# Performance work log

Measured on AMD Instinct MI355X. Metric: run time of the kernel, lower is better.

The kernel has to match this reference:

```python
import jax, jax.numpy as jnp
import numpy as np

N_NODES = 100000


def gcn_conv(x, W, b, src, dst, n):
    # PyG GCNConv: add self-loops, symmetric deg^-1/2 normalization,
    # transform then gather/scatter-add aggregate.
    loop = jnp.arange(n, dtype=src.dtype)
    s = jnp.concatenate([src, loop])
    d = jnp.concatenate([dst, loop])
    deg = jax.ops.segment_sum(jnp.ones_like(d, dtype=x.dtype), d, num_segments=n)
    dinv = jnp.where(deg > 0, 1.0 / jnp.sqrt(deg), 0.0)
    norm = dinv[s] * dinv[d]                      # [E+N]
    h = x @ W                                     # [N, out]
    msgs = h[s] * norm[:, None]                   # gather + scale
    out = jax.ops.segment_sum(msgs, d, num_segments=n)  # scatter-add
    return out + b


def setup_inputs() -> dict:
    key = jax.random.key(0)
    k1, k2, k3, k4 = jax.random.split(key, 4)
    F_in, H, D = 128, 16, 128
    x = jax.random.normal(k1, (N_NODES, F_in), dtype=jnp.float32)
    edge_index = jax.random.randint(k2, (2, 1600000), 0, N_NODES, dtype=jnp.int64)
    W1 = jax.random.normal(k3, (F_in, H), dtype=jnp.float32) / np.sqrt(F_in)
    b1 = jnp.zeros((H,), dtype=jnp.float32)
    W2 = jax.random.normal(k4, (H, D), dtype=jnp.float32) / np.sqrt(H)
    b2 = jnp.zeros((D,), dtype=jnp.float32)
    return {"x": x, "edge_index": edge_index, "W1": W1, "b1": b1, "W2": W2, "b2": b2}


def reference(x, edge_index, W1, b1, W2, b2):
    src, dst = edge_index[0], edge_index[1]
    n = x.shape[0]
    h = jax.nn.relu(gcn_conv(x, W1, b1, src, dst, n))
    out = jax.nn.relu(gcn_conv(h, W2, b2, src, dst, n))
    return out
```

## Files before the change

### kernel.cpp

```cpp
#include <hip/hip_runtime.h>
#include <hip/hip_fp16.h>
#include <stdint.h>

#define F_IN  128
#define HID   16
#define F_OUT 128
#define NBK   512
#define NBLK  512
#define BCAP  4096
#define CHUNK_MAX 4096
#define EPT   16
#define XP1   132
#define GT2_NODES 128

__device__ __forceinline__ int bucket_of(int d, int N) {
    return (int)(((long long)d * NBK) / N);
}
__device__ __forceinline__ int bucket_lo(int b, int N) {
    return (int)(((long long)b * N + NBK - 1) / NBK);
}

__global__ void __launch_bounds__(256) k_partf(
        const int* __restrict__ ei, int* __restrict__ bcur,
        uint32_t* __restrict__ pairs, int E, int N) {
    __shared__ int lh[NBK], lofs[NBK], lcur[NBK], gbase[NBK], lnlo[NBK];
    __shared__ int loff[256];
    __shared__ uint32_t spairs[CHUNK_MAX];
    __shared__ uint16_t sbkt[CHUNK_MAX];

    int blk = blockIdx.x, t = threadIdx.x;
    int C = (E + NBLK - 1) / NBLK;
    int e0 = blk * C;
    int e1 = e0 + C; if (e1 > E) e1 = E;
    int ecnt = e1 - e0;

    for (int i = t; i < NBK; i += 256) { lh[i] = 0; lnlo[i] = bucket_lo(i, N); }
    __syncthreads();

    int es[EPT], ed[EPT], eb[EPT];
#pragma unroll
    for (int k = 0; k < EPT; ++k) {
        int e = e0 + k * 256 + t;
        if (e < e1) {
            es[k] = ei[e];
            ed[k] = ei[E + e];
            eb[k] = bucket_of(ed[k], N);
            atomicAdd(&lh[eb[k]], 1);
        } else eb[k] = -1;
    }
    __syncthreads();

    int a0 = lh[2 * t], a1 = lh[2 * t + 1];
    int s2 = a0 + a1;
    loff[t] = s2;
    __syncthreads();
    for (int o = 1; o < 256; o <<= 1) {
        int a = (t >= o) ? loff[t - o] : 0;
        __syncthreads();
        loff[t] += a;
        __syncthreads();
    }
    int excl = loff[t] - s2;
    lofs[2 * t]     = excl;
    lofs[2 * t + 1] = excl + a0;
    lcur[2 * t]     = excl;
    lcur[2 * t + 1] = excl + a0;
    __syncthreads();

    for (int w = 0; w < NBK; w += 256) {
        int i = (t + w + blk) & (NBK - 1);
        int h = lh[i];
        gbase[i] = h ? atomicAdd(&bcur[i], h) : 0;
    }

#pragma unroll
    for (int k = 0; k < EPT; ++k) {
        if (eb[k] >= 0) {
            int b = eb[k];
            int idx = atomicAdd(&lcur[b], 1);
            spairs[idx] = ((uint32_t)es[k] << 10) | (uint32_t)(ed[k] - lnlo[b]);
            sbkt[idx]   = (uint16_t)b;
        }
    }
    __syncthreads();

    for (int i = t; i < ecnt; i += 256) {
        int b = sbkt[i];
        int pos = gbase[b] + (i - lofs[b]);
        if (pos < BCAP)
            pairs[(size_t)b * BCAP + pos] = spairs[i];
    }
}

__global__ void __launch_bounds__(256) k_csr_t1(
        const uint32_t* __restrict__ pairs, const int* __restrict__ bcur,
        const float* __restrict__ x, const float* __restrict__ W1,
        int* __restrict__ row_start, int* __restrict__ cnt,
        float* __restrict__ dinv, int* __restrict__ srcs,
        __half* __restrict__ g1, int N) {
    __shared__ union {
        struct { int lcnt[256]; int loff[256]; int lcur[256]; } c;
        struct { float sX[32 * XP1]; float sWt[HID * XP1]; } t1;
    } u;
    __shared__ float sdinv[224];

    int b = blockIdx.x, t = threadIdx.x;
    int base = b * BCAP;
    int ec = bcur[b]; if (ec > BCAP) ec = BCAP;
    int nlo = bucket_lo(b, N);
    int nhi = bucket_lo(b + 1, N); if (nhi > N) nhi = N;
    int nn = nhi - nlo;

    u.c.lcnt[t] = 0;
    __syncthreads();
    for (int e = t; e < ec; e += 256)
        atomicAdd(&u.c.lcnt[pairs[base + e] & 1023u], 1);
    __syncthreads();
    int v = u.c.lcnt[t];
    int pv = (v + 3) & ~3;
    u.c.loff[t] = pv;
    __syncthreads();
    for (int o = 1; o < 256; o <<= 1) {
        int a = (t >= o) ? u.c.loff[t - o] : 0;
        __syncthreads();
        u.c.loff[t] += a;
        __syncthreads();
    }
    if (t < nn) {
        int gs = base + (u.c.loff[t] - pv);
        row_start[nlo + t] = gs;
        cnt[nlo + t]       = v;
        float dv = rsqrtf((float)(v + 1));
        dinv[nlo + t]      = dv;
        sdinv[t]           = dv;
        u.c.lcur[t]        = gs;
    }
    __syncthreads();
    for (int e = t; e < ec; e += 256) {
        uint32_t p = pairs[base + e];
        int pos = atomicAdd(&u.c.lcur[p & 1023u], 1);
        srcs[pos] = (int)(p >> 10);
    }
    __syncthreads();

    for (int i = t; i < F_IN * HID; i += 256) {
        int k = i >> 4, f = i & 15;
        u.t1.sWt[f * XP1 + k] = W1[i];
    }
    int f  = t & 7;
    int nl = t >> 3;
    for (int c0 = 0; c0 < nn; c0 += 32) {
        __syncthreads();
        int node0 = nlo + c0;
        int nrem = nn - c0;
        const float4* x4 = (const float4*)(x + (size_t)node0 * F_IN);
#pragma unroll
        for (int j = 0; j < 4; ++j) {
            int idx4 = t + j * 256;
            int nl2 = idx4 >> 5;
            int kk = (idx4 & 31) * 4;
            float4 vv = make_float4(0.f, 0.f, 0.f, 0.f);
            if (nl2 < nrem) vv = x4[idx4];
            *(float4*)&u.t1.sX[nl2 * XP1 + kk] = vv;
        }
        __syncthreads();
        float a0 = 0.f, a1 = 0.f;
        const float* xr  = &u.t1.sX[nl * XP1];
        const float* wr0 = &u.t1.sWt[f * XP1];
        const float* wr1 = &u.t1.sWt[(f + 8) * XP1];
#pragma unroll 4
        for (int k = 0; k < F_IN; k += 4) {
            float4 xv = *(const float4*)(xr + k);
            float4 w0 = *(const float4*)(wr0 + k);
            float4 w1 = *(const float4*)(wr1 + k);
            a0 += xv.x * w0.x + xv.y * w0.y + xv.z * w0.z + xv.w * w0.w;
            a1 += xv.x * w1.x + xv.y * w1.y + xv.z * w1.z + xv.w * w1.w;
        }
        if (nl < nrem) {
            int node = node0 + nl;
            float di = sdinv[c0 + nl];
            g1[(size_t)node * HID + f]     = __float2half(di * a0);
            g1[(size_t)node * HID + f + 8] = __float2half(di * a1);
        }
    }
}

__device__ __forceinline__ void add_h8(float* __restrict__ acc, const __half* __restrict__ ptr) {
    uint4 u = *(const uint4*)ptr;
    const __half2* h = (const __half2*)&u;
#pragma unroll
    for (int q = 0; q < 4; ++q) {
        float2 f = __half22float2(h[q]);
        acc[2 * q]     += f.x;
        acc[2 * q + 1] += f.y;
    }
}

__device__ __forceinline__ void gather_acc(
        float* __restrict__ acc, int node, int p,
        const __half* __restrict__ g, const int* __restrict__ srcs,
        int rs, int deg) {
    {
        uint4 u = *(const uint4*)(g + (size_t)node * HID + p * 8);
        const __half2* h = (const __half2*)&u;
#pragma unroll
        for (int q = 0; q < 4; ++q) {
            float2 f = __half22float2(h[q]);
            acc[2 * q] = f.x; acc[2 * q + 1] = f.y;
        }
    }
    int j = 0;
    for (; j + 8 <= deg; j += 8) {
        int4 ia = *(const int4*)(srcs + rs + j);
        int4 ib = *(const int4*)(srcs + rs + j + 4);
        add_h8(acc, g + (size_t)ia.x * HID + p * 8);
        add_h8(acc, g + (size_t)ia.y * HID + p * 8);
        add_h8(acc, g + (size_t)ia.z * HID + p * 8);
        add_h8(acc, g + (size_t)ia.w * HID + p * 8);
        add_h8(acc, g + (size_t)ib.x * HID + p * 8);
        add_h8(acc, g + (size_t)ib.y * HID + p * 8);
        add_h8(acc, g + (size_t)ib.z * HID + p * 8);
        add_h8(acc, g + (size_t)ib.w * HID + p * 8);
    }
    if (j + 4 <= deg) {
        int4 ia = *(const int4*)(srcs + rs + j);
        add_h8(acc, g + (size_t)ia.x * HID + p * 8);
        add_h8(acc, g + (size_t)ia.y * HID + p * 8);
        add_h8(acc, g + (size_t)ia.z * HID + p * 8);
        add_h8(acc, g + (size_t)ia.w * HID + p * 8);
        j += 4;
    }
    for (; j < deg; ++j)
        add_h8(acc, g + (size_t)srcs[rs + j] * HID + p * 8);
}

__global__ void __launch_bounds__(256) k_gather1(
        const __half* __restrict__ g, const int* __restrict__ srcs,
        const int* __restrict__ row_start, const int* __restrict__ cnt,
        const float* __restrict__ dinv, const float* __restrict__ b1,
        __half* __restrict__ outb, int n) {
    int tt = blockIdx.x * 256 + threadIdx.x;
    int node = tt >> 1;
    int p = tt & 1;
    if (node >= n) return;
    float acc[8];
    gather_acc(acc, node, p, g, srcs, row_start[node], cnt[node]);
    float di = dinv[node];
#pragma unroll
    for (int i = 0; i < 8; ++i)
        acc[i] = di * fmaxf(di * acc[i] + b1[p * 8 + i], 0.0f);
    uint4 o;
    __half2* oh = (__half2*)&o;
#pragma unroll
    for (int q = 0; q < 4; ++q)
        oh[q] = __floats2half2_rn(acc[2 * q], acc[2 * q + 1]);
    *(uint4*)(outb + (size_t)node * HID + p * 8) = o;
}

__global__ void __launch_bounds__(256) k_gather_t2(
        const __half* __restrict__ g, const int* __restrict__ srcs,
        const int* __restrict__ row_start, const int* __restrict__ cnt,
        const float* __restrict__ dinv, const float* __restrict__ W2,
        const float* __restrict__ b2, float* __restrict__ out, int n) {
    __shared__ __half sAgg[GT2_NODES * HID];
    __shared__ float  sdv[GT2_NODES];
    int t = threadIdx.x;
    int node0 = blockIdx.x * GT2_NODES;

    {
        int nl = t >> 1, p = t & 1;
        int node = node0 + nl;
        if (node < n) {
            if (p == 0) sdv[nl] = dinv[node];
            float acc[8];
            gather_acc(acc, node, p, g, srcs, row_start[node], cnt[node]);
            uint4 o;
            __half2* oh = (__half2*)&o;
#pragma unroll
            for (int q = 0; q < 4; ++q)
                oh[q] = __floats2half2_rn(acc[2 * q], acc[2 * q + 1]);
            *(uint4*)&sAgg[nl * HID + p * 8] = o;
        }
    }
    __syncthreads();

    int d0 = (t & 31) * 4;
    int h  = t >> 5;
    float4 wcv[HID];
#pragma unroll
    for (int f2 = 0; f2 < HID; ++f2)
        wcv[f2] = *(const float4*)(W2 + f2 * F_OUT + d0);
    float4 bv = *(const float4*)(b2 + d0);
#pragma unroll 4
    for (int i = 0; i < GT2_NODES / 8; ++i) {
        int nl = h + 8 * i;
        int node = node0 + nl;
        if (node >= n) continue;
        const __half2* ah = (const __half2*)&sAgg[nl * HID];
        float4 s = make_float4(0.f, 0.f, 0.f, 0.f);
#pragma unroll
        for (int f2 = 0; f2 < HID; f2 += 2) {
            float2 fa = __half22float2(ah[f2 >> 1]);
            float4 w0 = wcv[f2], w1 = wcv[f2 + 1];
            s.x += fa.x * w0.x + fa.y * w1.x;
            s.y += fa.x * w0.y + fa.y * w1.y;
            s.z += fa.x * w0.z + fa.y * w1.z;
            s.w += fa.x * w0.w + fa.y * w1.w;
        }
        float dv = sdv[nl];
        float4 ov;
        ov.x = fmaxf(dv * s.x + bv.x, 0.f);
        ov.y = fmaxf(dv * s.y + bv.y, 0.f);
        ov.z = fmaxf(dv * s.z + bv.z, 0.f);
        ov.w = fmaxf(dv * s.w + bv.w, 0.f);
        *(float4*)(out + (size_t)node * F_OUT + d0) = ov;
    }
}

extern "C" void kernel_launch(void* const* d_in, const int* in_sizes, int n_in,
                              void* d_out, int out_size, void* d_ws, size_t ws_size,
                              hipStream_t stream) {
    const float* x  = (const float*)d_in[0];
    const int*   ei = (const int*)d_in[1];
    const float* W1 = (const float*)d_in[2];
    const float* b1 = (const float*)d_in[3];
    const float* W2 = (const float*)d_in[4];
    const float* b2 = (const float*)d_in[5];
    float* out = (float*)d_out;

    const int N = in_sizes[0] / F_IN;
    const int E = in_sizes[1] / 2;

    float* dinv      = (float*)d_ws;
    int*   cnt       = (int*)(dinv + N);
    int*   row_start = cnt + N;
    int*   bcur      = row_start + N;
    int*   srcs      = bcur + NBK;
    uint32_t* pairs  = (uint32_t*)(srcs + (size_t)NBK * BCAP);
    __half* bufA     = (__half*)(pairs + (size_t)NBK * BCAP);
    __half* bufB     = bufA + (size_t)N * HID;

    hipMemsetAsync(bcur, 0, NBK * sizeof(int), stream);
    k_partf<<<NBLK, 256, 0, stream>>>(ei, bcur, pairs, E, N);
    k_csr_t1<<<NBK, 256, 0, stream>>>(pairs, bcur, x, W1,
                                      row_start, cnt, dinv, srcs, bufA, N);
    k_gather1<<<((size_t)N * 2 + 255) / 256, 256, 0, stream>>>(
        bufA, srcs, row_start, cnt, dinv, b1, bufB, N);
    k_gather_t2<<<(N + GT2_NODES - 1) / GT2_NODES, 256, 0, stream>>>(
        bufB, srcs, row_start, cnt, dinv, W2, b2, out, N);
}
```

Before: 210.9 us.

## Split CSR build and X·W1 transform into separate kernels for more parallelism

The fused kernel that built per-bucket CSR and then ran the first linear transform over about 196 nodes serially per block is split in two. CSR construction stays at 512 blocks, and the transform becomes its own kernel with one block per 32 nodes, about 3125 blocks. The aim is to spread the x streaming and matmul across many more workgroups than 512. The cost is an extra kernel launch and reading dinv back from global memory.

```diff
diff --git a/kernel.cpp b/kernel.cpp
--- a/kernel.cpp
+++ b/kernel.cpp
@@ -92,96 +92,91 @@
     }
 }
 
-__global__ void __launch_bounds__(256) k_csr_t1(
+__global__ void __launch_bounds__(256) k_csr2(
         const uint32_t* __restrict__ pairs, const int* __restrict__ bcur,
-        const float* __restrict__ x, const float* __restrict__ W1,
         int* __restrict__ row_start, int* __restrict__ cnt,
-        float* __restrict__ dinv, int* __restrict__ srcs,
-        __half* __restrict__ g1, int N) {
-    __shared__ union {
-        struct { int lcnt[256]; int loff[256]; int lcur[256]; } c;
-        struct { float sX[32 * XP1]; float sWt[HID * XP1]; } t1;
-    } u;
-    __shared__ float sdinv[224];
-
+        float* __restrict__ dinv, int* __restrict__ srcs, int N) {
+    __shared__ int lcnt[256];
+    __shared__ int loff[256];
+    __shared__ int lcur[256];
     int b = blockIdx.x, t = threadIdx.x;
     int base = b * BCAP;
     int ec = bcur[b]; if (ec > BCAP) ec = BCAP;
     int nlo = bucket_lo(b, N);
     int nhi = bucket_lo(b + 1, N); if (nhi > N) nhi = N;
     int nn = nhi - nlo;
-
-    u.c.lcnt[t] = 0;
+    lcnt[t] = 0;
     __syncthreads();
     for (int e = t; e < ec; e += 256)
-        atomicAdd(&u.c.lcnt[pairs[base + e] & 1023u], 1);
-    __syncthreads();
-    int v = u.c.lcnt[t];
+        atomicAdd(&lcnt[pairs[base + e] & 1023u], 1);
+    __syncthreads();
+    int v = lcnt[t];
     int pv = (v + 3) & ~3;
-    u.c.loff[t] = pv;
+    loff[t] = pv;
     __syncthreads();
     for (int o = 1; o < 256; o <<= 1) {
-        int a = (t >= o) ? u.c.loff[t - o] : 0;
+        int a = (t >= o) ? loff[t - o] : 0;
         __syncthreads();
-        u.c.loff[t] += a;
+        loff[t] += a;
         __syncthreads();
     }
     if (t < nn) {
-        int gs = base + (u.c.loff[t] - pv);
+        int gs = base + (loff[t] - pv);
         row_start[nlo + t] = gs;
         cnt[nlo + t]       = v;
-        float dv = rsqrtf((float)(v + 1));
-        dinv[nlo + t]      = dv;
-        sdinv[t]           = dv;
-        u.c.lcur[t]        = gs;
+        dinv[nlo + t]      = rsqrtf((float)(v + 1));
+        lcur[t]            = gs;
     }
     __syncthreads();
     for (int e = t; e < ec; e += 256) {
         uint32_t p = pairs[base + e];
-        int pos = atomicAdd(&u.c.lcur[p & 1023u], 1);
+        int pos = atomicAdd(&lcur[p & 1023u], 1);
         srcs[pos] = (int)(p >> 10);
     }
-    __syncthreads();
-
+}
+
+__global__ void __launch_bounds__(256) k_transform1(
+        const float* __restrict__ x, const float* __restrict__ W1,
+        const float* __restrict__ dinv, __half* __restrict__ g1, int n) {
+    __shared__ float sX[32 * XP1];
+    __shared__ float sWt[HID * XP1];
+    int t = threadIdx.x;
+    int node0 = blockIdx.x * 32;
     for (int i = t; i < F_IN * HID; i += 256) {
         int k = i >> 4, f = i & 15;
-        u.t1.sWt[f * XP1 + k] = W1[i];
-    }
+        sWt[f * XP1 + k] = W1[i];
+    }
+    const float4* x4 = (const float4*)(x + (size_t)node0 * F_IN);
+    int nrem = n - node0;
+#pragma unroll
+    for (int j = 0; j < 4; ++j) {
+        int idx4 = t + j * 256;
+        int nl = idx4 >> 5;
+        int kk = (idx4 & 31) * 4;
+        float4 v = make_float4(0.f, 0.f, 0.f, 0.f);
+        if (nl < nrem) v = x4[idx4];
+        *(float4*)&sX[nl * XP1 + kk] = v;
+    }
+    __syncthreads();
     int f  = t & 7;
     int nl = t >> 3;
-    for (int c0 = 0; c0 < nn; c0 += 32) {
-        __syncthreads();
-        int node0 = nlo + c0;
-        int nrem = nn - c0;
-        const float4* x4 = (const float4*)(x + (size_t)node0 * F_IN);
-#pragma unroll
-        for (int j = 0; j < 4; ++j) {
-            int idx4 = t + j * 256;
-            int nl2 = idx4 >> 5;
-            int kk = (idx4 & 31) * 4;
-            float4 vv = make_float4(0.f, 0.f, 0.f, 0.f);
-            if (nl2 < nrem) vv = x4[idx4];
-            *(float4*)&u.t1.sX[nl2 * XP1 + kk] = vv;
-        }
-        __syncthreads();
-        float a0 = 0.f, a1 = 0.f;
-        const float* xr  = &u.t1.sX[nl * XP1];
-        const float* wr0 = &u.t1.sWt[f * XP1];
-        const float* wr1 = &u.t1.sWt[(f + 8) * XP1];
+    float a0 = 0.f, a1 = 0.f;
+    const float* xr  = &sX[nl * XP1];
+    const float* wr0 = &sWt[f * XP1];
+    const float* wr1 = &sWt[(f + 8) * XP1];
 #pragma unroll 4
-        for (int k = 0; k < F_IN; k += 4) {
-            float4 xv = *(const float4*)(xr + k);
-            float4 w0 = *(const float4*)(wr0 + k);
-            float4 w1 = *(const float4*)(wr1 + k);
-            a0 += xv.x * w0.x + xv.y * w0.y + xv.z * w0.z + xv.w * w0.w;
-            a1 += xv.x * w1.x + xv.y * w1.y + xv.z * w1.z + xv.w * w1.w;
-        }
-        if (nl < nrem) {
-            int node = node0 + nl;
-            float di = sdinv[c0 + nl];
-            g1[(size_t)node * HID + f]     = __float2half(di * a0);
-            g1[(size_t)node * HID + f + 8] = __float2half(di * a1);
-        }
+    for (int k = 0; k < F_IN; k += 4) {
+        float4 xv = *(const float4*)(xr + k);
+        float4 w0 = *(const float4*)(wr0 + k);
+        float4 w1 = *(const float4*)(wr1 + k);
+        a0 += xv.x * w0.x + xv.y * w0.y + xv.z * w0.z + xv.w * w0.w;
+        a1 += xv.x * w1.x + xv.y * w1.y + xv.z * w1.z + xv.w * w1.w;
+    }
+    int node = node0 + nl;
+    if (node < n) {
+        float di = dinv[node];
+        g1[(size_t)node * HID + f]     = __float2half(di * a0);
+        g1[(size_t)node * HID + f + 8] = __float2half(di * a1);
     }
 }
 
@@ -342,8 +337,8 @@
 
     hipMemsetAsync(bcur, 0, NBK * sizeof(int), stream);
     k_partf<<<NBLK, 256, 0, stream>>>(ei, bcur, pairs, E, N);
-    k_csr_t1<<<NBK, 256, 0, stream>>>(pairs, bcur, x, W1,
-                                      row_start, cnt, dinv, srcs, bufA, N);
+    k_csr2 <<<NBK, 256, 0, stream>>>(pairs, bcur, row_start, cnt, dinv, srcs, N);
+    k_transform1<<<(N + 31) / 32, 256, 0, stream>>>(x, W1, dinv, bufA, N);
     k_gather1<<<((size_t)N * 2 + 255) / 256, 256, 0, stream>>>(
         bufA, srcs, row_start, cnt, dinv, b1, bufB, N);
     k_gather_t2<<<(N + GT2_NODES - 1) / GT2_NODES, 256, 0, stream>>>(
```

Result: faster. 201.9 us (-4.3%).
